# Kernel optimization log

Measured on AMD Instinct MI355X. Metric: run time of the kernel, lower is better.

The kernel has to match this reference:

```python
import jax, jax.numpy as jnp
import numpy as np

GROUP = 9  # candidates per group, from .view(B, -1, 9)


def setup_inputs() -> dict:
    key = jax.random.key(0)
    k1, k2 = jax.random.split(key)
    x1 = jax.random.normal(k1, (8, 2048, 1024), dtype=jnp.float32)
    x2 = jax.random.normal(k2, (8, 1152, 1024), dtype=jnp.float32)
    return {"x1": x1, "x2": x2}


def reference(x1, x2):
    # batch pairwise squared distances: ||a||^2 + ||b||^2 - 2 a.b  -> [B, N1, N2]
    sq1 = jnp.sum(x1 * x1, axis=-1)[:, :, None]          # [B, N1, 1]
    sq2 = jnp.sum(x2 * x2, axis=-1)[:, None, :]          # [B, 1, N2]
    cross = jnp.einsum("bnd,bmd->bnm", x1, x2)           # [B, N1, N2]
    d = sq1 + sq2 - 2.0 * cross
    # group consecutive candidates in blocks of 9, mode='min'
    B = x1.shape[0]
    d = d.reshape(B, -1, GROUP)                           # [B, N1*N2/9, 9]
    d = jnp.min(d, axis=-1)                               # [B, N1*N2/9]
    # reduce=True -> scalar mean
    return jnp.mean(d)
```

## Files before the change

### kernel.cpp

```cpp
#include <hip/hip_runtime.h>
#include <hip/hip_bf16.h>

#define NB 8
#define N1 2048
#define N2 1152
#define KD 1024
#define BM 256
#define BN 144
#define BNP 145
#define BUFB 25600

typedef __attribute__((ext_vector_type(4))) float f32x4;
typedef __attribute__((ext_vector_type(2))) long i64x2;

__device__ __forceinline__ unsigned pack4_fp8(f32x4 v) {
  int t = __builtin_amdgcn_cvt_pk_fp8_f32(v.x, v.y, 0, false);
  t = __builtin_amdgcn_cvt_pk_fp8_f32(v.z, v.w, t, true);
  return (unsigned)t;
}

__global__ __launch_bounds__(256) void convert_kernel(
    const float* __restrict__ x1, const float* __restrict__ x2,
    unsigned char* __restrict__ x1q, unsigned char* __restrict__ x2q,
    float* __restrict__ sq1, float* __restrict__ sq2) {
  __shared__ __align__(16) unsigned char lds[4096];
  int wave = threadIdx.x >> 6, lane = threadIdx.x & 63;
  int bid = blockIdx.x;
  int b = bid & 7;
  int idx = bid >> 3;
  const float* src;
  unsigned char* dst;
  float* sqp;
  if (idx < N1 / 4) {
    int row = b * N1 + idx * 4 + wave;
    src = x1 + (size_t)row * KD;
    dst = x1q + (size_t)row * KD;
    sqp = sq1 + row;
  } else {
    int row = b * N2 + (idx - N1 / 4) * 4 + wave;
    src = x2 + (size_t)row * KD;
    dst = x2q + (size_t)row * KD;
    sqp = sq2 + row;
  }
  const f32x4* s4 = (const f32x4*)src;
  int r = 4 * (lane & 15);
  int q = (r & 31) >> 3;
  int h = r >> 5;
  int pos = (lane >> 4) * 64 + q * 16 + h * 8 + (r & 7);
  unsigned char* my = lds + wave * 1024;
  float s = 0.f;
#pragma unroll
  for (int i = 0; i < 4; ++i) {
    f32x4 v = __builtin_nontemporal_load(&s4[i * 64 + lane]);
    *(unsigned*)(my + i * 256 + pos) = pack4_fp8(v);
    s += v.x * v.x + v.y * v.y + v.z * v.z + v.w * v.w;
  }
  __syncthreads();
  ((uint4*)dst)[lane] = *(const uint4*)(my + lane * 16);
#pragma unroll
  for (int off = 32; off > 0; off >>= 1) s += __shfl_down(s, off);
  if (lane == 0) *sqp = s;
}

__device__ __forceinline__ void async_copy16(const void* g, void* l) {
  __builtin_amdgcn_global_load_lds(
      (const __attribute__((address_space(1))) unsigned int*)g,
      (__attribute__((address_space(3))) unsigned int*)l, 16, 0, 0);
}

__global__ __launch_bounds__(256, 2) void dist_kernel(
    const unsigned char* __restrict__ x1q, const unsigned char* __restrict__ x2q,
    const float* __restrict__ sq1, const float* __restrict__ sq2,
    float* __restrict__ out) {
  __shared__ __align__(16) char smem[2 * BUFB];

  const int tid = threadIdx.x;
  const int wave = tid >> 6, lane = tid & 63;
  const int bid = blockIdx.x;
  const int b = bid & 7;
  const int bm = (bid >> 3) & 7;
  const int bn = bid >> 6;

  const unsigned char* Ag = x1q + ((size_t)b * N1 + bm * BM) * KD;
  const unsigned char* Bg = x2q + ((size_t)b * N2 + bn * BN) * KD;

  const int lr = lane >> 2, sl = lane & 3;
  const int goff = (sl ^ ((lr >> 1) & 3)) * 16;

  const int quad = lane >> 4, fr = lane & 15;
  const int fslot = (fr * 4 + (quad ^ ((fr >> 1) & 3))) * 16;

  f32x4 acc[4][9];
#pragma unroll
  for (int i = 0; i < 4; ++i)
#pragma unroll
    for (int j = 0; j < 9; ++j) {
      f32x4 z = {0.f, 0.f, 0.f, 0.f};
      acc[i][j] = z;
    }

  auto stage = [&](int buf, int k0) {
    char* base = smem + buf * BUFB;
    for (int j = wave; j < 25; j += 4) {
      const unsigned char* g;
      if (j < 16)
        g = Ag + (size_t)(j * 16 + lr) * KD + k0 + goff;
      else
        g = Bg + (size_t)((j - 16) * 16 + lr) * KD + k0 + goff;
      async_copy16(g, base + j * 1024 + lane * 16);
    }
  };

  stage(0, 0);
  for (int i = 0; i < 16; ++i) {
    const int cur = i & 1;
    __syncthreads();
    if (i < 15) stage(cur ^ 1, (i + 1) * 64);
    const char* cb = smem + cur * BUFB;

    i64x2 a[4];
#pragma unroll
    for (int tm = 0; tm < 4; ++tm)
      a[tm] = *(const i64x2*)(cb + (wave * 4 + tm) * 1024 + fslot);
#pragma unroll
    for (int tn = 0; tn < 9; ++tn) {
      i64x2 bf = *(const i64x2*)(cb + 16384 + tn * 1024 + fslot);
#pragma unroll
      for (int tm = 0; tm < 4; ++tm) {
        acc[tm][tn] = __builtin_amdgcn_mfma_f32_16x16x32_fp8_fp8(a[tm].x, bf.x, acc[tm][tn], 0, 0, 0);
        acc[tm][tn] = __builtin_amdgcn_mfma_f32_16x16x32_fp8_fp8(a[tm].y, bf.y, acc[tm][tn], 0, 0, 0);
      }
    }
  }

  float s2[9];
#pragma unroll
  for (int tn = 0; tn < 9; ++tn)
    s2[tn] = sq2[(size_t)b * N2 + bn * BN + tn * 16 + fr];

  float s1v[4][4];
#pragma unroll
  for (int tm = 0; tm < 4; ++tm)
#pragma unroll
    for (int r = 0; r < 4; ++r)
      s1v[tm][r] = sq1[(size_t)b * N1 + bm * BM + wave * 64 + tm * 16 + quad * 4 + r];

  float* eps = (float*)smem;
  float local = 0.f;
#pragma unroll
  for (int tm = 0; tm < 4; ++tm) {
    __syncthreads();
#pragma unroll
    for (int tn = 0; tn < 9; ++tn)
#pragma unroll
      for (int r = 0; r < 4; ++r)
        eps[(wave * 16 + quad * 4 + r) * BNP + tn * 16 + fr] =
            s1v[tm][r] + s2[tn] - 2.0f * acc[tm][tn][r];
    __syncthreads();
#pragma unroll
    for (int qq = 0; qq < 4; ++qq) {
      int g = tid + qq * 256;
      int row = g >> 4, grp = g & 15;
      const float* p = eps + row * BNP + grp * 9;
      float mn = p[0];
#pragma unroll
      for (int jj = 1; jj < 9; ++jj) mn = fminf(mn, p[jj]);
      local += mn;
    }
  }

#pragma unroll
  for (int off = 32; off > 0; off >>= 1) local += __shfl_down(local, off);
  __syncthreads();
  if (lane == 0) eps[wave] = local;
  __syncthreads();
  if (tid == 0) {
    float s = eps[0] + eps[1] + eps[2] + eps[3];
    atomicAdd(out, s * (1.0f / 2097152.0f));
  }
}

extern "C" void kernel_launch(void* const* d_in, const int* in_sizes, int n_in,
                              void* d_out, int out_size, void* d_ws, size_t ws_size,
                              hipStream_t stream) {
  const float* x1 = (const float*)d_in[0];
  const float* x2 = (const float*)d_in[1];
  char* ws = (char*)d_ws;
  const size_t x1q_bytes = (size_t)NB * N1 * KD;
  const size_t x2q_bytes = (size_t)NB * N2 * KD;
  unsigned char* x1q = (unsigned char*)ws;
  unsigned char* x2q = (unsigned char*)(ws + x1q_bytes);
  float* sq1 = (float*)(ws + x1q_bytes + x2q_bytes);
  float* sq2 = (float*)(ws + x1q_bytes + x2q_bytes + (size_t)NB * N1 * 4);

  (void)hipMemsetAsync(d_out, 0, sizeof(float), stream);
  convert_kernel<<<NB * (N1 / 4 + N2 / 4), 256, 0, stream>>>(x1, x2, x1q, x2q, sq1, sq2);
  dist_kernel<<<NB * (N1 / BM) * (N2 / BN), 256, 0, stream>>>(x1q, x2q, sq1, sq2,
                                                              (float*)d_out);
}
```

Measured before the change: 155.8 us.

## Fuse fp8 conversion and distance GEMM into one kernel with grid barrier

Merges the fp32-to-fp8 conversion and the distance/min/mean kernel into a single persistent launch of 512 blocks. Each block first converts 50 rows, then all blocks meet at a global atomic barrier before the MFMA GEMM phase. The output zeroing moves from a memset into the last block to arrive. This removes one kernel launch and the gap between the two kernels, but relies on all 512 blocks being resident at once (2 per CU on 256 CUs) or the barrier deadlocks. The convert phase also runs at lower parallelism than the old standalone kernel.

Measured after the change: 274.3 us. 76.1% more time.

```diff
diff --git a/kernel.cpp b/kernel.cpp
--- a/kernel.cpp
+++ b/kernel.cpp
@@ -1,5 +1,4 @@
 #include <hip/hip_runtime.h>
-#include <hip/hip_bf16.h>
 
 #define NB 8
 #define N1 2048
@@ -9,6 +8,8 @@
 #define BN 144
 #define BNP 145
 #define BUFB 25600
+#define GRID (NB * (N1 / BM) * (N2 / BN))
+#define BAR_OFF 26316800
 
 typedef __attribute__((ext_vector_type(4))) float f32x4;
 typedef __attribute__((ext_vector_type(2))) long i64x2;
@@ -19,65 +20,90 @@
   return (unsigned)t;
 }
 
-__global__ __launch_bounds__(256) void convert_kernel(
-    const float* __restrict__ x1, const float* __restrict__ x2,
-    unsigned char* __restrict__ x1q, unsigned char* __restrict__ x2q,
-    float* __restrict__ sq1, float* __restrict__ sq2) {
-  __shared__ __align__(16) unsigned char lds[4096];
-  int wave = threadIdx.x >> 6, lane = threadIdx.x & 63;
-  int bid = blockIdx.x;
-  int b = bid & 7;
-  int idx = bid >> 3;
-  const float* src;
-  unsigned char* dst;
-  float* sqp;
-  if (idx < N1 / 4) {
-    int row = b * N1 + idx * 4 + wave;
-    src = x1 + (size_t)row * KD;
-    dst = x1q + (size_t)row * KD;
-    sqp = sq1 + row;
-  } else {
-    int row = b * N2 + (idx - N1 / 4) * 4 + wave;
-    src = x2 + (size_t)row * KD;
-    dst = x2q + (size_t)row * KD;
-    sqp = sq2 + row;
-  }
-  const f32x4* s4 = (const f32x4*)src;
-  int r = 4 * (lane & 15);
-  int q = (r & 31) >> 3;
-  int h = r >> 5;
-  int pos = (lane >> 4) * 64 + q * 16 + h * 8 + (r & 7);
-  unsigned char* my = lds + wave * 1024;
-  float s = 0.f;
-#pragma unroll
-  for (int i = 0; i < 4; ++i) {
-    f32x4 v = __builtin_nontemporal_load(&s4[i * 64 + lane]);
-    *(unsigned*)(my + i * 256 + pos) = pack4_fp8(v);
-    s += v.x * v.x + v.y * v.y + v.z * v.z + v.w * v.w;
-  }
-  __syncthreads();
-  ((uint4*)dst)[lane] = *(const uint4*)(my + lane * 16);
-#pragma unroll
-  for (int off = 32; off > 0; off >>= 1) s += __shfl_down(s, off);
-  if (lane == 0) *sqp = s;
-}
-
 __device__ __forceinline__ void async_copy16(const void* g, void* l) {
   __builtin_amdgcn_global_load_lds(
       (const __attribute__((address_space(1))) unsigned int*)g,
       (__attribute__((address_space(3))) unsigned int*)l, 16, 0, 0);
 }
 
-__global__ __launch_bounds__(256, 2) void dist_kernel(
-    const unsigned char* __restrict__ x1q, const unsigned char* __restrict__ x2q,
-    const float* __restrict__ sq1, const float* __restrict__ sq2,
-    float* __restrict__ out) {
+__global__ __launch_bounds__(256, 2) void fused_kernel(
+    const float* __restrict__ x1, const float* __restrict__ x2,
+    unsigned char* __restrict__ x1q, unsigned char* __restrict__ x2q,
+    float* __restrict__ sq1, float* __restrict__ sq2,
+    float* __restrict__ out, unsigned* __restrict__ bar) {
   __shared__ __align__(16) char smem[2 * BUFB];
 
   const int tid = threadIdx.x;
   const int wave = tid >> 6, lane = tid & 63;
   const int bid = blockIdx.x;
   const int b = bid & 7;
+
+  {
+    const int base = (bid >> 3) * 50;
+    unsigned char* my = (unsigned char*)smem + wave * 1024;
+    const int r = 4 * (lane & 15);
+    const int q = (r & 31) >> 3;
+    const int h = r >> 5;
+    const int pos = (lane >> 4) * 64 + q * 16 + h * 8 + (r & 7);
+    for (int t = 0; t < 13; ++t) {
+      const int ri = t * 4 + wave;
+      const int rr = base + ri;
+      const float* src = nullptr;
+      unsigned char* dst = nullptr;
+      float* sqp = nullptr;
+      if (ri < 50) {
+        if (rr < N1) {
+          const int row = b * N1 + rr;
+          src = x1 + (size_t)row * KD;
+          dst = x1q + (size_t)row * KD;
+          sqp = sq1 + row;
+        } else {
+          const int row = b * N2 + (rr - N1);
+          src = x2 + (size_t)row * KD;
+          dst = x2q + (size_t)row * KD;
+          sqp = sq2 + row;
+        }
+      }
+      float s = 0.f;
+      if (ri < 50) {
+        const f32x4* s4 = (const f32x4*)src;
+#pragma unroll
+        for (int i2 = 0; i2 < 4; ++i2) {
+          f32x4 v = __builtin_nontemporal_load(&s4[i2 * 64 + lane]);
+          *(unsigned*)(my + i2 * 256 + pos) = pack4_fp8(v);
+          s += v.x * v.x + v.y * v.y + v.z * v.z + v.w * v.w;
+        }
+      }
+      __syncthreads();
+      if (ri < 50) {
+        ((uint4*)dst)[lane] = *(const uint4*)(my + lane * 16);
+#pragma unroll
+        for (int off = 32; off > 0; off >>= 1) s += __shfl_down(s, off);
+        if (lane == 0) *sqp = s;
+      }
+    }
+  }
+
+  __threadfence();
+  __syncthreads();
+  if (tid == 0) {
+    unsigned old = __hip_atomic_fetch_add(&bar[0], 1u, __ATOMIC_ACQ_REL,
+                                          __HIP_MEMORY_SCOPE_AGENT);
+    if (old == GRID - 1) {
+      atomicExch(out, 0.0f);
+      __threadfence();
+      __hip_atomic_store(&bar[1], 1u, __ATOMIC_RELEASE,
+                         __HIP_MEMORY_SCOPE_AGENT);
+    } else {
+      while (__hip_atomic_load(&bar[1], __ATOMIC_ACQUIRE,
+                               __HIP_MEMORY_SCOPE_AGENT) == 0u) {
+        __builtin_amdgcn_s_sleep(2);
+      }
+    }
+  }
+  __syncthreads();
+  __threadfence();
+
   const int bm = (bid >> 3) & 7;
   const int bn = bid >> 6;
 
@@ -142,8 +168,8 @@
 #pragma unroll
   for (int tm = 0; tm < 4; ++tm)
 #pragma unroll
-    for (int r = 0; r < 4; ++r)
-      s1v[tm][r] = sq1[(size_t)b * N1 + bm * BM + wave * 64 + tm * 16 + quad * 4 + r];
+    for (int rr = 0; rr < 4; ++rr)
+      s1v[tm][rr] = sq1[(size_t)b * N1 + bm * BM + wave * 64 + tm * 16 + quad * 4 + rr];
 
   float* eps = (float*)smem;
   float local = 0.f;
@@ -153,9 +179,9 @@
 #pragma unroll
     for (int tn = 0; tn < 9; ++tn)
 #pragma unroll
-      for (int r = 0; r < 4; ++r)
-        eps[(wave * 16 + quad * 4 + r) * BNP + tn * 16 + fr] =
-            s1v[tm][r] + s2[tn] - 2.0f * acc[tm][tn][r];
+      for (int rr = 0; rr < 4; ++rr)
+        eps[(wave * 16 + quad * 4 + rr) * BNP + tn * 16 + fr] =
+            s1v[tm][rr] + s2[tn] - 2.0f * acc[tm][tn][rr];
     __syncthreads();
 #pragma unroll
     for (int qq = 0; qq < 4; ++qq) {
@@ -192,9 +218,9 @@
   unsigned char* x2q = (unsigned char*)(ws + x1q_bytes);
   float* sq1 = (float*)(ws + x1q_bytes + x2q_bytes);
   float* sq2 = (float*)(ws + x1q_bytes + x2q_bytes + (size_t)NB * N1 * 4);
-
-  (void)hipMemsetAsync(d_out, 0, sizeof(float), stream);
-  convert_kernel<<<NB * (N1 / 4 + N2 / 4), 256, 0, stream>>>(x1, x2, x1q, x2q, sq1, sq2);
-  dist_kernel<<<NB * (N1 / BM) * (N2 / BN), 256, 0, stream>>>(x1q, x2q, sq1, sq2,
-                                                              (float*)d_out);
-}
+  unsigned* bar = (unsigned*)(ws + BAR_OFF);
+
+  (void)hipMemsetAsync(bar, 0, 2 * sizeof(unsigned), stream);
+  fused_kernel<<<GRID, 256, 0, stream>>>(x1, x2, x1q, x2q, sq1, sq2,
+                                         (float*)d_out, bar);
+}
```

## Triple-buffer dist kernel loads with vmcnt waits and fold output zeroing into convert

Applied to the files above, without the earlier changes.

The dist kernel's LDS staging goes from double to triple buffering. Loads are prefetched two k-steps ahead, and explicit s_waitcnt vmcnt/lgkmcnt plus a raw s_barrier replace __syncthreads, so loads can stay in flight across iterations. Each wave's staging work becomes a fixed unrolled set of 6 copies plus one shared extra copy. The separate hipMemsetAsync is dropped and the output is zeroed by convert_kernel instead, saving one launch. The LDS footprint grows to about 75KB per block, which may limit occupancy against the requested two blocks per CU, and the hand-counted vmcnt(7) must match the number of copies issued per stage.

Result: faster. 150.7 us (-3.3%).

```diff
diff --git a/kernel.cpp b/kernel.cpp
--- a/kernel.cpp
+++ b/kernel.cpp
@@ -1,5 +1,4 @@
 #include <hip/hip_runtime.h>
-#include <hip/hip_bf16.h>
 
 #define NB 8
 #define N1 2048
@@ -9,6 +8,7 @@
 #define BN 144
 #define BNP 145
 #define BUFB 25600
+#define NBUF 3
 
 typedef __attribute__((ext_vector_type(4))) float f32x4;
 typedef __attribute__((ext_vector_type(2))) long i64x2;
@@ -19,11 +19,19 @@
   return (unsigned)t;
 }
 
+__device__ __forceinline__ void async_copy16(const void* g, void* l) {
+  __builtin_amdgcn_global_load_lds(
+      (const __attribute__((address_space(1))) unsigned int*)g,
+      (__attribute__((address_space(3))) unsigned int*)l, 16, 0, 0);
+}
+
 __global__ __launch_bounds__(256) void convert_kernel(
     const float* __restrict__ x1, const float* __restrict__ x2,
     unsigned char* __restrict__ x1q, unsigned char* __restrict__ x2q,
-    float* __restrict__ sq1, float* __restrict__ sq2) {
+    float* __restrict__ sq1, float* __restrict__ sq2,
+    float* __restrict__ out) {
   __shared__ __align__(16) unsigned char lds[4096];
+  if (blockIdx.x == 0 && threadIdx.x == 0) *out = 0.f;
   int wave = threadIdx.x >> 6, lane = threadIdx.x & 63;
   int bid = blockIdx.x;
   int b = bid & 7;
@@ -62,17 +70,11 @@
   if (lane == 0) *sqp = s;
 }
 
-__device__ __forceinline__ void async_copy16(const void* g, void* l) {
-  __builtin_amdgcn_global_load_lds(
-      (const __attribute__((address_space(1))) unsigned int*)g,
-      (__attribute__((address_space(3))) unsigned int*)l, 16, 0, 0);
-}
-
 __global__ __launch_bounds__(256, 2) void dist_kernel(
     const unsigned char* __restrict__ x1q, const unsigned char* __restrict__ x2q,
     const float* __restrict__ sq1, const float* __restrict__ sq2,
     float* __restrict__ out) {
-  __shared__ __align__(16) char smem[2 * BUFB];
+  __shared__ __align__(16) char smem[NBUF * BUFB];
 
   const int tid = threadIdx.x;
   const int wave = tid >> 6, lane = tid & 63;
@@ -101,7 +103,9 @@
 
   auto stage = [&](int buf, int k0) {
     char* base = smem + buf * BUFB;
-    for (int j = wave; j < 25; j += 4) {
+#pragma unroll
+    for (int t = 0; t < 6; ++t) {
+      int j = wave * 6 + t;
       const unsigned char* g;
       if (j < 16)
         g = Ag + (size_t)(j * 16 + lr) * KD + k0 + goff;
@@ -109,29 +113,50 @@
         g = Bg + (size_t)((j - 16) * 16 + lr) * KD + k0 + goff;
       async_copy16(g, base + j * 1024 + lane * 16);
     }
+    async_copy16(Bg + (size_t)(128 + lr) * KD + k0 + goff,
+                 base + 24 * 1024 + lane * 16);
   };
 
+#define COMPUTE(cbp)                                                          \
+  {                                                                           \
+    const char* cb = (cbp);                                                   \
+    i64x2 a[4];                                                               \
+    _Pragma("unroll") for (int tm = 0; tm < 4; ++tm)                          \
+        a[tm] = *(const i64x2*)(cb + (wave * 4 + tm) * 1024 + fslot);         \
+    _Pragma("unroll") for (int tn = 0; tn < 9; ++tn) {                        \
+      i64x2 bf = *(const i64x2*)(cb + 16384 + tn * 1024 + fslot);             \
+      _Pragma("unroll") for (int tm = 0; tm < 4; ++tm) {                      \
+        acc[tm][tn] = __builtin_amdgcn_mfma_f32_16x16x32_fp8_fp8(             \
+            a[tm].x, bf.x, acc[tm][tn], 0, 0, 0);                             \
+        acc[tm][tn] = __builtin_amdgcn_mfma_f32_16x16x32_fp8_fp8(             \
+            a[tm].y, bf.y, acc[tm][tn], 0, 0, 0);                             \
+      }                                                                       \
+    }                                                                         \
+  }
+
   stage(0, 0);
-  for (int i = 0; i < 16; ++i) {
-    const int cur = i & 1;
-    __syncthreads();
-    if (i < 15) stage(cur ^ 1, (i + 1) * 64);
-    const char* cb = smem + cur * BUFB;
-
-    i64x2 a[4];
-#pragma unroll
-    for (int tm = 0; tm < 4; ++tm)
-      a[tm] = *(const i64x2*)(cb + (wave * 4 + tm) * 1024 + fslot);
-#pragma unroll
-    for (int tn = 0; tn < 9; ++tn) {
-      i64x2 bf = *(const i64x2*)(cb + 16384 + tn * 1024 + fslot);
-#pragma unroll
-      for (int tm = 0; tm < 4; ++tm) {
-        acc[tm][tn] = __builtin_amdgcn_mfma_f32_16x16x32_fp8_fp8(a[tm].x, bf.x, acc[tm][tn], 0, 0, 0);
-        acc[tm][tn] = __builtin_amdgcn_mfma_f32_16x16x32_fp8_fp8(a[tm].y, bf.y, acc[tm][tn], 0, 0, 0);
-      }
-    }
-  }
+  stage(1, 64);
+
+  int cur = 0;
+  for (int i = 0; i < 15; ++i) {
+    asm volatile("s_waitcnt lgkmcnt(0)" ::: "memory");
+    asm volatile("s_waitcnt vmcnt(7)" ::: "memory");
+    __builtin_amdgcn_s_barrier();
+    __builtin_amdgcn_sched_barrier(0);
+    if (i < 14) {
+      int b2 = cur + 2;
+      if (b2 >= NBUF) b2 -= NBUF;
+      stage(b2, (i + 2) * 64);
+    }
+    COMPUTE(smem + cur * BUFB);
+    ++cur;
+    if (cur == NBUF) cur = 0;
+  }
+  asm volatile("s_waitcnt lgkmcnt(0)" ::: "memory");
+  asm volatile("s_waitcnt vmcnt(0)" ::: "memory");
+  __builtin_amdgcn_s_barrier();
+  __builtin_amdgcn_sched_barrier(0);
+  COMPUTE(smem + cur * BUFB);
 
   float s2[9];
 #pragma unroll
@@ -142,8 +167,8 @@
 #pragma unroll
   for (int tm = 0; tm < 4; ++tm)
 #pragma unroll
-    for (int r = 0; r < 4; ++r)
-      s1v[tm][r] = sq1[(size_t)b * N1 + bm * BM + wave * 64 + tm * 16 + quad * 4 + r];
+    for (int rr = 0; rr < 4; ++rr)
+      s1v[tm][rr] = sq1[(size_t)b * N1 + bm * BM + wave * 64 + tm * 16 + quad * 4 + rr];
 
   float* eps = (float*)smem;
   float local = 0.f;
@@ -153,9 +178,9 @@
 #pragma unroll
     for (int tn = 0; tn < 9; ++tn)
 #pragma unroll
-      for (int r = 0; r < 4; ++r)
-        eps[(wave * 16 + quad * 4 + r) * BNP + tn * 16 + fr] =
-            s1v[tm][r] + s2[tn] - 2.0f * acc[tm][tn][r];
+      for (int rr = 0; rr < 4; ++rr)
+        eps[(wave * 16 + quad * 4 + rr) * BNP + tn * 16 + fr] =
+            s1v[tm][rr] + s2[tn] - 2.0f * acc[tm][tn][rr];
     __syncthreads();
 #pragma unroll
     for (int qq = 0; qq < 4; ++qq) {
@@ -193,8 +218,9 @@
   float* sq1 = (float*)(ws + x1q_bytes + x2q_bytes);
   float* sq2 = (float*)(ws + x1q_bytes + x2q_bytes + (size_t)NB * N1 * 4);
 
-  (void)hipMemsetAsync(d_out, 0, sizeof(float), stream);
-  convert_kernel<<<NB * (N1 / 4 + N2 / 4), 256, 0, stream>>>(x1, x2, x1q, x2q, sq1, sq2);
+  convert_kernel<<<NB * (N1 / 4 + N2 / 4), 256, 0, stream>>>(x1, x2, x1q, x2q,
+                                                             sq1, sq2,
+                                                             (float*)d_out);
   dist_kernel<<<NB * (N1 / BM) * (N2 / BN), 256, 0, stream>>>(x1q, x2q, sq1, sq2,
                                                               (float*)d_out);
 }
```
